# Optimization experiments

Measured on AMD Instinct MI355X. Metric: run time of the kernel, lower is better.

Reference implementation:

```python
import jax, jax.numpy as jnp
import numpy as np

N = 100000
E = 200000
SD = 128   # structural_dim
CD = 768   # chemical_dim


def _linear_params(key, fan_in, fan_out):
    kw, kb = jax.random.split(key)
    bound = 1.0 / np.sqrt(fan_in)
    W = jax.random.uniform(kw, (fan_in, fan_out), jnp.float32, -bound, bound)
    b = jax.random.uniform(kb, (fan_out,), jnp.float32, -bound, bound)
    return W, b


def setup_inputs() -> dict:
    key = jax.random.key(0)
    ks = jax.random.split(key, 12)
    z = jax.random.normal(ks[0], (N, SD), jnp.float32)
    chemistry = jax.random.normal(ks[1], (N, CD), jnp.float32)
    edge = jax.random.randint(ks[2], (E, 2), 0, N, jnp.int64)
    smiles_mask = jax.random.randint(ks[3], (N,), 0, 2, jnp.int32)
    # structural_mlp: SD -> SD//2 -> 1
    sw1, sb1 = _linear_params(ks[4], SD, SD // 2)
    sw2, sb2 = _linear_params(ks[5], SD // 2, 1)
    # chemical_mlp: CD -> CD//4 -> 1
    cw1, cb1 = _linear_params(ks[6], CD, CD // 4)
    cw2, cb2 = _linear_params(ks[7], CD // 4, 1)
    # combined_mlp: SD+CD -> SD -> 1
    mw1, mb1 = _linear_params(ks[8], SD + CD, SD)
    mw2, mb2 = _linear_params(ks[9], SD, 1)
    path_weights = jnp.ones((3,), jnp.float32) / 3.0
    return dict(z=z, chemistry=chemistry, edge=edge, smiles_mask=smiles_mask,
                sw1=sw1, sb1=sb1, sw2=sw2, sb2=sb2,
                cw1=cw1, cb1=cb1, cw2=cw2, cb2=cb2,
                mw1=mw1, mb1=mb1, mw2=mw2, mb2=mb2,
                path_weights=path_weights)


def reference(z, chemistry, edge, smiles_mask,
              sw1, sb1, sw2, sb2,
              cw1, cb1, cw2, cb2,
              mw1, mb1, mw2, mb2,
              path_weights):
    src, dst = edge[:, 0], edge[:, 1]
    # per-edge gathers + elementwise products
    structural_prod = z[src] * z[dst]                    # [E, SD]
    chemical_prod = chemistry[src] * chemistry[dst]      # [E, CD]
    # three small MLPs (dropout is identity in eval mode)
    score_structural = (jax.nn.relu(structural_prod @ sw1 + sb1) @ sw2 + sb2)[:, 0]
    score_chemical = (jax.nn.relu(chemical_prod @ cw1 + cb1) @ cw2 + cb2)[:, 0]
    combined_prod = jnp.concatenate([structural_prod, chemical_prod], axis=-1)  # [E, SD+CD]
    score_combined = (jax.nn.relu(combined_prod @ mw1 + mb1) @ mw2 + mb2)[:, 0]
    # fixed learned path weights (use_gating=False)
    w = jax.nn.softmax(path_weights)
    scores = w[0] * score_structural + w[1] * score_chemical + w[2] * score_combined
    # fall back to structural-only score where chemistry is missing on either end
    mask = smiles_mask.astype(z.dtype)
    both_valid = mask[src] * mask[dst]
    return jnp.where(both_valid > 0.5, scores, score_structural)  # [E]
```

## Files before the change

kernel.cpp:

```cpp
#include <hip/hip_runtime.h>


typedef float  f32x4  __attribute__((ext_vector_type(4)));
typedef __bf16 bf16x8 __attribute__((ext_vector_type(8)));
typedef unsigned short u16x4 __attribute__((ext_vector_type(4)));

static_assert(sizeof(bf16x8) == 16, "bf16x8 must be 16B");
static_assert(sizeof(f32x4) == 16, "f32x4 must be 16B");

#define N_NODES 100000
#define E_EDGES 200000
#define KSTEPS  28
#define NOUT    384
#define PTOT    (KSTEPS * NOUT * 32)

#define WS_WHI   0
#define WS_WLO   688128
#define WS_B1    1376256
#define WS_W2    1377792
#define WS_CONST 1379328

__device__ __forceinline__ unsigned short f2bf(float f) {
  unsigned int x = __float_as_uint(f);
  unsigned int r = (x + 0x7FFFu + ((x >> 16) & 1u)) >> 16;
  return (unsigned short)r;
}
__device__ __forceinline__ float bf2f(unsigned short u) {
  return __uint_as_float(((unsigned int)u) << 16);
}

__global__ __launch_bounds__(256) void prep_kernel(
    const float* __restrict__ sw1, const float* __restrict__ sb1,
    const float* __restrict__ sw2, const float* __restrict__ sb2,
    const float* __restrict__ cw1, const float* __restrict__ cb1,
    const float* __restrict__ cw2, const float* __restrict__ cb2,
    const float* __restrict__ mw1, const float* __restrict__ mb1,
    const float* __restrict__ mw2, const float* __restrict__ mb2,
    const float* __restrict__ pw,  const int* __restrict__ edge_i32,
    unsigned short* __restrict__ whi, unsigned short* __restrict__ wlo,
    float* __restrict__ b1cat, float* __restrict__ w2cat,
    float* __restrict__ consts)
{
  const int idx = blockIdx.x * 256 + threadIdx.x;
  if (idx < PTOT) {
    const int p  = idx / (NOUT * 32);
    const int r  = idx % (NOUT * 32);
    const int n  = r >> 5;
    const int kk = r & 31;
    const int k  = p * 32 + kk;
    float v;
    if (n < 64)       v = (k < 128)  ? sw1[k * 64 + n] : 0.0f;
    else if (n < 256) v = (k >= 128) ? cw1[(size_t)(k - 128) * 192 + (n - 64)] : 0.0f;
    else              v = mw1[(size_t)k * 128 + (n - 256)];
    const unsigned short hi = f2bf(v);
    const unsigned short lo = f2bf(v - bf2f(hi));
    whi[idx] = hi;
    wlo[idx] = lo;
  } else if (idx < PTOT + NOUT) {
    const int j = idx - PTOT;
    float b, w;
    if (j < 64)       { b = sb1[j];       w = sw2[j]; }
    else if (j < 256) { b = cb1[j - 64];  w = cw2[j - 64]; }
    else              { b = mb1[j - 256]; w = mw2[j - 256]; }
    b1cat[j] = b;
    w2cat[j] = w;
  } else if (idx == PTOT + NOUT) {
    const float p0 = pw[0], p1 = pw[1], p2 = pw[2];
    const float mx = fmaxf(p0, fmaxf(p1, p2));
    const float e0 = __expf(p0 - mx), e1 = __expf(p1 - mx), e2 = __expf(p2 - mx);
    const float inv = 1.0f / (e0 + e1 + e2);
    const float w0 = e0 * inv, w1 = e1 * inv, w2v = e2 * inv;
    consts[0] = w0; consts[1] = w1; consts[2] = w2v;
    consts[3] = w0 * sb2[0] + w1 * cb2[0] + w2v * mb2[0];
    consts[4] = sb2[0];
    unsigned o = 0;
    for (int i = 0; i < 64; ++i) o |= (unsigned)edge_i32[2 * i + 1];
    consts[5] = (o == 0u) ? 1.0f : 0.0f;
  }
}

__global__ __launch_bounds__(256, 2) void decoder_main(
    const float* __restrict__ z, const float* __restrict__ chem,
    const int* __restrict__ edge, const int* __restrict__ mask,
    const unsigned short* __restrict__ whi, const unsigned short* __restrict__ wlo,
    const float* __restrict__ b1cat, const float* __restrict__ w2cat,
    const float* __restrict__ consts, float* __restrict__ out)
{
  __shared__ unsigned short Ah[2][64][40];
  __shared__ unsigned short Al[2][64][40];
  __shared__ int   srcL[64];
  __shared__ int   dstL[64];
  __shared__ float validL[64];
  __shared__ float scoreL[64];

  const int tid  = threadIdx.x;
  const int lane = tid & 63;
  const int wv   = tid >> 6;
  const int li   = lane & 15;
  const int q    = lane >> 4;
  const int m0   = blockIdx.x << 6;

  if (tid < 64) {
    scoreL[tid] = 0.0f;
    const int e = m0 + tid;
    int s_, d_;
    if (consts[5] > 0.5f) { s_ = edge[4 * e]; d_ = edge[4 * e + 2]; }
    else                  { s_ = edge[2 * e]; d_ = edge[2 * e + 1]; }
    srcL[tid] = s_;
    dstL[tid] = d_;
    validL[tid] = (mask[s_] != 0 && mask[d_] != 0) ? 1.0f : 0.0f;
  }
  __syncthreads();

  const int mA = tid >> 3;
  const int mB = 32 + mA;
  const int kc = (tid & 7) << 2;
  const float* zsA = z + (size_t)srcL[mA] * 128 + kc;
  const float* zdA = z + (size_t)dstL[mA] * 128 + kc;
  const float* zsB = z + (size_t)srcL[mB] * 128 + kc;
  const float* zdB = z + (size_t)dstL[mB] * 128 + kc;
  const float* csA = chem + (size_t)srcL[mA] * 768 + kc;
  const float* cdA = chem + (size_t)dstL[mA] * 768 + kc;
  const float* csB = chem + (size_t)srcL[mB] * 768 + kc;
  const float* cdB = chem + (size_t)dstL[mB] * 768 + kc;

  auto split_store = [&](int buf, int m, f32x4 p) {
    u16x4 h, l;
#pragma unroll
    for (int j = 0; j < 4; ++j) {
      const unsigned short hj = f2bf(p[j]);
      h[j] = hj;
      l[j] = f2bf(p[j] - bf2f(hj));
    }
    *(u16x4*)&Ah[buf][m][kc] = h;
    *(u16x4*)&Al[buf][m][kc] = l;
  };

  {
    const f32x4 a0 = *(const f32x4*)zsA;
    const f32x4 b0 = *(const f32x4*)zdA;
    const f32x4 a1 = *(const f32x4*)zsB;
    const f32x4 b1 = *(const f32x4*)zdB;
    split_store(0, mA, a0 * b0);
    split_store(0, mB, a1 * b1);
  }
  __syncthreads();

  f32x4 acc[4][6];
#pragma unroll
  for (int mt = 0; mt < 4; ++mt)
#pragma unroll
    for (int i = 0; i < 6; ++i)
      acc[mt][i] = (f32x4){0.f, 0.f, 0.f, 0.f};

  for (int s = 0; s < KSTEPS; ++s) {
    const int buf = s & 1;

    bf16x8 afh[4], afl[4];
#pragma unroll
    for (int mt = 0; mt < 4; ++mt) {
      afh[mt] = *(const bf16x8*)&Ah[buf][mt * 16 + li][q * 8];
      afl[mt] = *(const bf16x8*)&Al[buf][mt * 16 + li][q * 8];
    }

    bf16x8 bfh[6], bfl[6];
    bool act[6];
#pragma unroll
    for (int i = 0; i < 6; ++i) {
      const int ti = wv + 4 * i;
      const int path = (ti < 4) ? 0 : (ti < 16 ? 1 : 2);
      act[i] = (path == 0) ? (s < 4) : (path == 1) ? (s >= 4) : true;
      if (act[i]) {
        const size_t off = (size_t)s * (NOUT * 32) + (size_t)(ti * 16 + li) * 32 + q * 8;
        bfh[i] = *(const bf16x8*)(whi + off);
        bfl[i] = *(const bf16x8*)(wlo + off);
      }
    }

    f32x4 ga, gb, gc, gd;
    if (s + 1 < KSTEPS) {
      const int k0 = (s + 1) * 32;
      if (k0 < 128) {
        ga = *(const f32x4*)(zsA + k0); gb = *(const f32x4*)(zdA + k0);
        gc = *(const f32x4*)(zsB + k0); gd = *(const f32x4*)(zdB + k0);
      } else {
        const int ko = k0 - 128;
        ga = *(const f32x4*)(csA + ko); gb = *(const f32x4*)(cdA + ko);
        gc = *(const f32x4*)(csB + ko); gd = *(const f32x4*)(cdB + ko);
      }
    }

#pragma unroll
    for (int i = 0; i < 6; ++i) {
      if (act[i]) {
#pragma unroll
        for (int mt = 0; mt < 4; ++mt) {
          acc[mt][i] = __builtin_amdgcn_mfma_f32_16x16x32_bf16(afh[mt], bfh[i], acc[mt][i], 0, 0, 0);
          acc[mt][i] = __builtin_amdgcn_mfma_f32_16x16x32_bf16(afh[mt], bfl[i], acc[mt][i], 0, 0, 0);
          acc[mt][i] = __builtin_amdgcn_mfma_f32_16x16x32_bf16(afl[mt], bfh[i], acc[mt][i], 0, 0, 0);
        }
      }
    }

    if (s + 1 < KSTEPS) {
      const int nbuf = buf ^ 1;
      split_store(nbuf, mA, ga * gb);
      split_store(nbuf, mB, gc * gd);
    }
    __syncthreads();
  }

  float part[4][4];
#pragma unroll
  for (int mt = 0; mt < 4; ++mt)
#pragma unroll
    for (int r = 0; r < 4; ++r) part[mt][r] = 0.f;

  const float w0c = consts[0], w1c = consts[1], w2c = consts[2];
#pragma unroll
  for (int i = 0; i < 6; ++i) {
    const int ti = wv + 4 * i;
    const int path = (ti < 4) ? 0 : (ti < 16 ? 1 : 2);
    const int col = ti * 16 + li;
    const float b1 = b1cat[col];
    const float w2 = w2cat[col];
    const float wp  = (path == 0) ? w0c : (path == 1) ? w1c : w2c;
    const float p0f = (path == 0) ? 1.0f : 0.0f;
#pragma unroll
    for (int mt = 0; mt < 4; ++mt) {
#pragma unroll
      for (int r = 0; r < 4; ++r) {
        const float valid = validL[mt * 16 + q * 4 + r];
        const float a = p0f + valid * (wp - p0f);
        float v = acc[mt][i][r] + b1;
        v = fmaxf(v, 0.0f);
        part[mt][r] += a * v * w2;
      }
    }
  }

#pragma unroll
  for (int mt = 0; mt < 4; ++mt) {
#pragma unroll
    for (int r = 0; r < 4; ++r) {
      float v = part[mt][r];
      v += __shfl_xor(v, 1);
      v += __shfl_xor(v, 2);
      v += __shfl_xor(v, 4);
      v += __shfl_xor(v, 8);
      if (li == 0) atomicAdd(&scoreL[mt * 16 + q * 4 + r], v);
    }
  }
  __syncthreads();

  if (tid < 64) {
    const float valid = validL[tid];
    const float cadd = consts[4] + valid * (consts[3] - consts[4]);
    out[m0 + tid] = scoreL[tid] + cadd;
  }
}

extern "C" void kernel_launch(void* const* d_in, const int* in_sizes, int n_in,
                              void* d_out, int out_size, void* d_ws, size_t ws_size,
                              hipStream_t stream)
{
  const float* z    = (const float*)d_in[0];
  const float* chem = (const float*)d_in[1];
  const int*   edge = (const int*)d_in[2];
  const int*   mask = (const int*)d_in[3];
  const float* sw1  = (const float*)d_in[4];
  const float* sb1  = (const float*)d_in[5];
  const float* sw2  = (const float*)d_in[6];
  const float* sb2  = (const float*)d_in[7];
  const float* cw1  = (const float*)d_in[8];
  const float* cb1  = (const float*)d_in[9];
  const float* cw2  = (const float*)d_in[10];
  const float* cb2  = (const float*)d_in[11];
  const float* mw1  = (const float*)d_in[12];
  const float* mb1  = (const float*)d_in[13];
  const float* mw2  = (const float*)d_in[14];
  const float* mb2  = (const float*)d_in[15];
  const float* pw   = (const float*)d_in[16];

  char* ws = (char*)d_ws;
  unsigned short* whi = (unsigned short*)(ws + WS_WHI);
  unsigned short* wlo = (unsigned short*)(ws + WS_WLO);
  float* b1cat  = (float*)(ws + WS_B1);
  float* w2cat  = (float*)(ws + WS_W2);
  float* consts = (float*)(ws + WS_CONST);

  const int prep_tasks  = PTOT + NOUT + 64;
  const int prep_blocks = (prep_tasks + 255) / 256;
  prep_kernel<<<prep_blocks, 256, 0, stream>>>(
      sw1, sb1, sw2, sb2, cw1, cb1, cw2, cb2, mw1, mb1, mw2, mb2, pw, edge,
      whi, wlo, b1cat, w2cat, consts);

  decoder_main<<<E_EDGES / 64, 256, 0, stream>>>(
      z, chem, edge, mask, whi, wlo, b1cat, w2cat, consts, (float*)d_out);
}
```

Measured before the change: 761.5 us.

## Rewrite decoder as single-wave fp16 split-A kernel without LDS staging

```diff
diff --git a/kernel.cpp b/kernel.cpp
--- a/kernel.cpp
+++ b/kernel.cpp
@@ -1,33 +1,19 @@
 #include <hip/hip_runtime.h>
 
 
-typedef float  f32x4  __attribute__((ext_vector_type(4)));
-typedef __bf16 bf16x8 __attribute__((ext_vector_type(8)));
-typedef unsigned short u16x4 __attribute__((ext_vector_type(4)));
-
-static_assert(sizeof(bf16x8) == 16, "bf16x8 must be 16B");
-static_assert(sizeof(f32x4) == 16, "f32x4 must be 16B");
-
-#define N_NODES 100000
+typedef float    f32x4 __attribute__((ext_vector_type(4)));
+typedef _Float16 f16x8 __attribute__((ext_vector_type(8)));
+
 #define E_EDGES 200000
 #define KSTEPS  28
 #define NOUT    384
 #define PTOT    (KSTEPS * NOUT * 32)
-
-#define WS_WHI   0
-#define WS_WLO   688128
-#define WS_B1    1376256
-#define WS_W2    1377792
-#define WS_CONST 1379328
-
-__device__ __forceinline__ unsigned short f2bf(float f) {
-  unsigned int x = __float_as_uint(f);
-  unsigned int r = (x + 0x7FFFu + ((x >> 16) & 1u)) >> 16;
-  return (unsigned short)r;
-}
-__device__ __forceinline__ float bf2f(unsigned short u) {
-  return __uint_as_float(((unsigned int)u) << 16);
-}
+#define PANEL   (NOUT * 32)
+
+#define WS_WH    0
+#define WS_B1    688128
+#define WS_W2    (688128 + 1536)
+#define WS_CONST (688128 + 3072)
 
 __global__ __launch_bounds__(256) void prep_kernel(
     const float* __restrict__ sw1, const float* __restrict__ sb1,
@@ -37,14 +23,14 @@
     const float* __restrict__ mw1, const float* __restrict__ mb1,
     const float* __restrict__ mw2, const float* __restrict__ mb2,
     const float* __restrict__ pw,  const int* __restrict__ edge_i32,
-    unsigned short* __restrict__ whi, unsigned short* __restrict__ wlo,
+    _Float16* __restrict__ wh,
     float* __restrict__ b1cat, float* __restrict__ w2cat,
     float* __restrict__ consts)
 {
   const int idx = blockIdx.x * 256 + threadIdx.x;
   if (idx < PTOT) {
-    const int p  = idx / (NOUT * 32);
-    const int r  = idx % (NOUT * 32);
+    const int p  = idx / PANEL;
+    const int r  = idx % PANEL;
     const int n  = r >> 5;
     const int kk = r & 31;
     const int k  = p * 32 + kk;
@@ -52,10 +38,7 @@
     if (n < 64)       v = (k < 128)  ? sw1[k * 64 + n] : 0.0f;
     else if (n < 256) v = (k >= 128) ? cw1[(size_t)(k - 128) * 192 + (n - 64)] : 0.0f;
     else              v = mw1[(size_t)k * 128 + (n - 256)];
-    const unsigned short hi = f2bf(v);
-    const unsigned short lo = f2bf(v - bf2f(hi));
-    whi[idx] = hi;
-    wlo[idx] = lo;
+    wh[idx] = (_Float16)v;
   } else if (idx < PTOT + NOUT) {
     const int j = idx - PTOT;
     float b, w;
@@ -79,184 +62,213 @@
   }
 }
 
-__global__ __launch_bounds__(256, 2) void decoder_main(
+#define FMA2(ACC, AH, AL, B)                                              \
+  ACC = __builtin_amdgcn_mfma_f32_16x16x32_f16(AH, B, ACC, 0, 0, 0);      \
+  ACC = __builtin_amdgcn_mfma_f32_16x16x32_f16(AL, B, ACC, 0, 0, 0);
+
+__global__ __launch_bounds__(64, 2) void decoder_main(
     const float* __restrict__ z, const float* __restrict__ chem,
     const int* __restrict__ edge, const int* __restrict__ mask,
-    const unsigned short* __restrict__ whi, const unsigned short* __restrict__ wlo,
+    const _Float16* __restrict__ wh,
     const float* __restrict__ b1cat, const float* __restrict__ w2cat,
     const float* __restrict__ consts, float* __restrict__ out)
 {
-  __shared__ unsigned short Ah[2][64][40];
-  __shared__ unsigned short Al[2][64][40];
-  __shared__ int   srcL[64];
-  __shared__ int   dstL[64];
-  __shared__ float validL[64];
-  __shared__ float scoreL[64];
-
-  const int tid  = threadIdx.x;
-  const int lane = tid & 63;
-  const int wv   = tid >> 6;
+  const int lane = threadIdx.x;
   const int li   = lane & 15;
   const int q    = lane >> 4;
-  const int m0   = blockIdx.x << 6;
-
-  if (tid < 64) {
-    scoreL[tid] = 0.0f;
-    const int e = m0 + tid;
-    int s_, d_;
-    if (consts[5] > 0.5f) { s_ = edge[4 * e]; d_ = edge[4 * e + 2]; }
-    else                  { s_ = edge[2 * e]; d_ = edge[2 * e + 1]; }
-    srcL[tid] = s_;
-    dstL[tid] = d_;
-    validL[tid] = (mask[s_] != 0 && mask[d_] != 0) ? 1.0f : 0.0f;
-  }
-  __syncthreads();
-
-  const int mA = tid >> 3;
-  const int mB = 32 + mA;
-  const int kc = (tid & 7) << 2;
-  const float* zsA = z + (size_t)srcL[mA] * 128 + kc;
-  const float* zdA = z + (size_t)dstL[mA] * 128 + kc;
-  const float* zsB = z + (size_t)srcL[mB] * 128 + kc;
-  const float* zdB = z + (size_t)dstL[mB] * 128 + kc;
-  const float* csA = chem + (size_t)srcL[mA] * 768 + kc;
-  const float* cdA = chem + (size_t)dstL[mA] * 768 + kc;
-  const float* csB = chem + (size_t)srcL[mB] * 768 + kc;
-  const float* cdB = chem + (size_t)dstL[mB] * 768 + kc;
-
-  auto split_store = [&](int buf, int m, f32x4 p) {
-    u16x4 h, l;
-#pragma unroll
-    for (int j = 0; j < 4; ++j) {
-      const unsigned short hj = f2bf(p[j]);
-      h[j] = hj;
-      l[j] = f2bf(p[j] - bf2f(hj));
-    }
-    *(u16x4*)&Ah[buf][m][kc] = h;
-    *(u16x4*)&Al[buf][m][kc] = l;
-  };
-
-  {
-    const f32x4 a0 = *(const f32x4*)zsA;
-    const f32x4 b0 = *(const f32x4*)zdA;
-    const f32x4 a1 = *(const f32x4*)zsB;
-    const f32x4 b1 = *(const f32x4*)zdB;
-    split_store(0, mA, a0 * b0);
-    split_store(0, mB, a1 * b1);
-  }
-  __syncthreads();
-
-  f32x4 acc[4][6];
-#pragma unroll
-  for (int mt = 0; mt < 4; ++mt)
-#pragma unroll
-    for (int i = 0; i < 6; ++i)
-      acc[mt][i] = (f32x4){0.f, 0.f, 0.f, 0.f};
-
-  for (int s = 0; s < KSTEPS; ++s) {
-    const int buf = s & 1;
-
-    bf16x8 afh[4], afl[4];
-#pragma unroll
-    for (int mt = 0; mt < 4; ++mt) {
-      afh[mt] = *(const bf16x8*)&Ah[buf][mt * 16 + li][q * 8];
-      afl[mt] = *(const bf16x8*)&Al[buf][mt * 16 + li][q * 8];
-    }
-
-    bf16x8 bfh[6], bfl[6];
-    bool act[6];
-#pragma unroll
-    for (int i = 0; i < 6; ++i) {
-      const int ti = wv + 4 * i;
-      const int path = (ti < 4) ? 0 : (ti < 16 ? 1 : 2);
-      act[i] = (path == 0) ? (s < 4) : (path == 1) ? (s >= 4) : true;
-      if (act[i]) {
-        const size_t off = (size_t)s * (NOUT * 32) + (size_t)(ti * 16 + li) * 32 + q * 8;
-        bfh[i] = *(const bf16x8*)(whi + off);
-        bfl[i] = *(const bf16x8*)(wlo + off);
+  const int kq   = q * 8;
+  const int base = blockIdx.x * 32;
+
+  const int e0 = base + li;
+  const int e1 = base + 16 + li;
+  int s0, d0, s1, d1;
+  if (consts[5] > 0.5f) {
+    s0 = edge[4 * e0]; d0 = edge[4 * e0 + 2];
+    s1 = edge[4 * e1]; d1 = edge[4 * e1 + 2];
+  } else {
+    s0 = edge[2 * e0]; d0 = edge[2 * e0 + 1];
+    s1 = edge[2 * e1]; d1 = edge[2 * e1 + 1];
+  }
+  const float v0 = (mask[s0] != 0 && mask[d0] != 0) ? 1.0f : 0.0f;
+  const float v1 = (mask[s1] != 0 && mask[d1] != 0) ? 1.0f : 0.0f;
+
+  const float* zs0 = z + (size_t)s0 * 128 + kq;
+  const float* zd0 = z + (size_t)d0 * 128 + kq;
+  const float* zs1 = z + (size_t)s1 * 128 + kq;
+  const float* zd1 = z + (size_t)d1 * 128 + kq;
+  const float* cs0 = chem + (size_t)s0 * 768 + kq;
+  const float* cd0 = chem + (size_t)d0 * 768 + kq;
+  const float* cs1 = chem + (size_t)s1 * 768 + kq;
+  const float* cd1 = chem + (size_t)d1 * 768 + kq;
+
+  f32x4 gs0a, gs0b, gd0a, gd0b, gs1a, gs1b, gd1a, gd1b;
+#define LD8(P, OFF, A, B)                        \
+  A = *(const f32x4*)((P) + (OFF));              \
+  B = *(const f32x4*)((P) + (OFF) + 4);
+
+#define MKFRAG(SA, SB, DA, DB, AH, AL)           \
+  {                                              \
+    _Pragma("unroll")                            \
+    for (int j = 0; j < 4; ++j) {                \
+      const float p  = (SA)[j] * (DA)[j];        \
+      const _Float16 h = (_Float16)p;            \
+      (AH)[j] = h;                               \
+      (AL)[j] = (_Float16)(p - (float)h);        \
+      const float p2 = (SB)[j] * (DB)[j];        \
+      const _Float16 h2 = (_Float16)p2;          \
+      (AH)[4 + j] = h2;                          \
+      (AL)[4 + j] = (_Float16)(p2 - (float)h2);  \
+    }                                            \
+  }
+
+#define BFRAG(S, TI) \
+  (*(const f16x8*)(wh + (size_t)(S) * PANEL + ((TI) * 16 + li) * 32 + q * 8))
+
+  const float w0c = consts[0], w1c = consts[1], w2c = consts[2];
+
+  float part[2][4];
+#pragma unroll
+  for (int mt = 0; mt < 2; ++mt)
+#pragma unroll
+    for (int r = 0; r < 4; ++r) part[mt][r] = 0.0f;
+
+#define RETIRE(ACC, TI, MT, WVALID, WINVALID)                              \
+  {                                                                        \
+    const int col = (TI) * 16 + li;                                        \
+    const float b1 = b1cat[col];                                           \
+    const float w2 = w2cat[col];                                           \
+    _Pragma("unroll")                                                      \
+    for (int r = 0; r < 4; ++r) {                                          \
+      const float vld = __shfl((MT) ? v1 : v0, q * 4 + r);                 \
+      const float a = (WINVALID) + vld * ((WVALID) - (WINVALID));          \
+      part[MT][r] += a * fmaxf((ACC)[r] + b1, 0.0f) * w2;                  \
+    }                                                                      \
+  }
+
+  f32x4 accS[4][2], accC[8][2];
+#pragma unroll
+  for (int t = 0; t < 4; ++t) {
+    accS[t][0] = (f32x4){0.f, 0.f, 0.f, 0.f};
+    accS[t][1] = (f32x4){0.f, 0.f, 0.f, 0.f};
+  }
+#pragma unroll
+  for (int t = 0; t < 8; ++t) {
+    accC[t][0] = (f32x4){0.f, 0.f, 0.f, 0.f};
+    accC[t][1] = (f32x4){0.f, 0.f, 0.f, 0.f};
+  }
+
+  LD8(zs0, 0, gs0a, gs0b) LD8(zd0, 0, gd0a, gd0b)
+  LD8(zs1, 0, gs1a, gs1b) LD8(zd1, 0, gd1a, gd1b)
+
+#pragma unroll
+  for (int s = 0; s < 4; ++s) {
+    f16x8 a0h, a0l, a1h, a1l;
+    MKFRAG(gs0a, gs0b, gd0a, gd0b, a0h, a0l)
+    MKFRAG(gs1a, gs1b, gd1a, gd1b, a1h, a1l)
+
+    if (s < 3) {
+      const int off = (s + 1) * 32;
+      LD8(zs0, off, gs0a, gs0b) LD8(zd0, off, gd0a, gd0b)
+      LD8(zs1, off, gs1a, gs1b) LD8(zd1, off, gd1a, gd1b)
+    } else {
+      LD8(cs0, 0, gs0a, gs0b) LD8(cd0, 0, gd0a, gd0b)
+      LD8(cs1, 0, gs1a, gs1b) LD8(cd1, 0, gd1a, gd1b)
+    }
+
+#pragma unroll
+    for (int t = 0; t < 4; ++t) {
+      const f16x8 b = BFRAG(s, t);
+      FMA2(accS[t][0], a0h, a0l, b)
+      FMA2(accS[t][1], a1h, a1l, b)
+    }
+#pragma unroll
+    for (int t = 0; t < 8; ++t) {
+      const f16x8 b = BFRAG(s, 16 + t);
+      FMA2(accC[t][0], a0h, a0l, b)
+      FMA2(accC[t][1], a1h, a1l, b)
+    }
+  }
+
+#pragma unroll
+  for (int t = 0; t < 4; ++t) {
+    RETIRE(accS[t][0], t, 0, w0c, 1.0f)
+    RETIRE(accS[t][1], t, 1, w0c, 1.0f)
+  }
+
+  f32x4 accH[12][2];
+#pragma unroll
+  for (int t = 0; t < 12; ++t) {
+    accH[t][0] = (f32x4){0.f, 0.f, 0.f, 0.f};
+    accH[t][1] = (f32x4){0.f, 0.f, 0.f, 0.f};
+  }
+
+  for (int s = 4; s < KSTEPS; ++s) {
+    f16x8 a0h, a0l, a1h, a1l;
+    MKFRAG(gs0a, gs0b, gd0a, gd0b, a0h, a0l)
+    MKFRAG(gs1a, gs1b, gd1a, gd1b, a1h, a1l)
+
+    if (s + 1 < KSTEPS) {
+      const int off = (s + 1) * 32 - 128;
+      LD8(cs0, off, gs0a, gs0b) LD8(cd0, off, gd0a, gd0b)
+      LD8(cs1, off, gs1a, gs1b) LD8(cd1, off, gd1a, gd1b)
+    }
+
+#pragma unroll
+    for (int t = 0; t < 12; ++t) {
+      const f16x8 b = BFRAG(s, 4 + t);
+      FMA2(accH[t][0], a0h, a0l, b)
+      FMA2(accH[t][1], a1h, a1l, b)
+    }
+#pragma unroll
+    for (int t = 0; t < 8; ++t) {
+      const f16x8 b = BFRAG(s, 16 + t);
+      FMA2(accC[t][0], a0h, a0l, b)
+      FMA2(accC[t][1], a1h, a1l, b)
+    }
+  }
+
+#pragma unroll
+  for (int t = 0; t < 12; ++t) {
+    RETIRE(accH[t][0], 4 + t, 0, w1c, 0.0f)
+    RETIRE(accH[t][1], 4 + t, 1, w1c, 0.0f)
+  }
+#pragma unroll
+  for (int t = 0; t < 8; ++t) {
+    RETIRE(accC[t][0], 16 + t, 0, w2c, 0.0f)
+    RETIRE(accC[t][1], 16 + t, 1, w2c, 0.0f)
+  }
+
+#pragma unroll
+  for (int mt = 0; mt < 2; ++mt) {
+#pragma unroll
+    for (int r = 0; r < 4; ++r) {
+      float vv = part[mt][r];
+      vv += __shfl_xor(vv, 1);
+      vv += __shfl_xor(vv, 2);
+      vv += __shfl_xor(vv, 4);
+      vv += __shfl_xor(vv, 8);
+      part[mt][r] = vv;
+    }
+  }
+
+  const float c3 = consts[3], c4 = consts[4];
+  float outv[2][4];
+#pragma unroll
+  for (int mt = 0; mt < 2; ++mt) {
+#pragma unroll
+    for (int r = 0; r < 4; ++r) {
+      const float vld = __shfl(mt ? v1 : v0, q * 4 + r);
+      outv[mt][r] = part[mt][r] + c4 + vld * (c3 - c4);
+    }
+  }
+  if (li == 0) {
+#pragma unroll
+    for (int mt = 0; mt < 2; ++mt) {
+#pragma unroll
+      for (int r = 0; r < 4; ++r) {
+        out[base + mt * 16 + q * 4 + r] = outv[mt][r];
       }
     }
-
-    f32x4 ga, gb, gc, gd;
-    if (s + 1 < KSTEPS) {
-      const int k0 = (s + 1) * 32;
-      if (k0 < 128) {
-        ga = *(const f32x4*)(zsA + k0); gb = *(const f32x4*)(zdA + k0);
-        gc = *(const f32x4*)(zsB + k0); gd = *(const f32x4*)(zdB + k0);
-      } else {
-        const int ko = k0 - 128;
-        ga = *(const f32x4*)(csA + ko); gb = *(const f32x4*)(cdA + ko);
-        gc = *(const f32x4*)(csB + ko); gd = *(const f32x4*)(cdB + ko);
-      }
-    }
-
-#pragma unroll
-    for (int i = 0; i < 6; ++i) {
-      if (act[i]) {
-#pragma unroll
-        for (int mt = 0; mt < 4; ++mt) {
-          acc[mt][i] = __builtin_amdgcn_mfma_f32_16x16x32_bf16(afh[mt], bfh[i], acc[mt][i], 0, 0, 0);
-          acc[mt][i] = __builtin_amdgcn_mfma_f32_16x16x32_bf16(afh[mt], bfl[i], acc[mt][i], 0, 0, 0);
-          acc[mt][i] = __builtin_amdgcn_mfma_f32_16x16x32_bf16(afl[mt], bfh[i], acc[mt][i], 0, 0, 0);
-        }
-      }
-    }
-
-    if (s + 1 < KSTEPS) {
-      const int nbuf = buf ^ 1;
-      split_store(nbuf, mA, ga * gb);
-      split_store(nbuf, mB, gc * gd);
-    }
-    __syncthreads();
-  }
-
-  float part[4][4];
-#pragma unroll
-  for (int mt = 0; mt < 4; ++mt)
-#pragma unroll
-    for (int r = 0; r < 4; ++r) part[mt][r] = 0.f;
-
-  const float w0c = consts[0], w1c = consts[1], w2c = consts[2];
-#pragma unroll
-  for (int i = 0; i < 6; ++i) {
-    const int ti = wv + 4 * i;
-    const int path = (ti < 4) ? 0 : (ti < 16 ? 1 : 2);
-    const int col = ti * 16 + li;
-    const float b1 = b1cat[col];
-    const float w2 = w2cat[col];
-    const float wp  = (path == 0) ? w0c : (path == 1) ? w1c : w2c;
-    const float p0f = (path == 0) ? 1.0f : 0.0f;
-#pragma unroll
-    for (int mt = 0; mt < 4; ++mt) {
-#pragma unroll
-      for (int r = 0; r < 4; ++r) {
-        const float valid = validL[mt * 16 + q * 4 + r];
-        const float a = p0f + valid * (wp - p0f);
-        float v = acc[mt][i][r] + b1;
-        v = fmaxf(v, 0.0f);
-        part[mt][r] += a * v * w2;
-      }
-    }
-  }
-
-#pragma unroll
-  for (int mt = 0; mt < 4; ++mt) {
-#pragma unroll
-    for (int r = 0; r < 4; ++r) {
-      float v = part[mt][r];
-      v += __shfl_xor(v, 1);
-      v += __shfl_xor(v, 2);
-      v += __shfl_xor(v, 4);
-      v += __shfl_xor(v, 8);
-      if (li == 0) atomicAdd(&scoreL[mt * 16 + q * 4 + r], v);
-    }
-  }
-  __syncthreads();
-
-  if (tid < 64) {
-    const float valid = validL[tid];
-    const float cadd = consts[4] + valid * (consts[3] - consts[4]);
-    out[m0 + tid] = scoreL[tid] + cadd;
   }
 }
 
@@ -283,8 +295,7 @@
   const float* pw   = (const float*)d_in[16];
 
   char* ws = (char*)d_ws;
-  unsigned short* whi = (unsigned short*)(ws + WS_WHI);
-  unsigned short* wlo = (unsigned short*)(ws + WS_WLO);
+  _Float16* wh  = (_Float16*)(ws + WS_WH);
   float* b1cat  = (float*)(ws + WS_B1);
   float* w2cat  = (float*)(ws + WS_W2);
   float* consts = (float*)(ws + WS_CONST);
@@ -293,8 +304,8 @@
   const int prep_blocks = (prep_tasks + 255) / 256;
   prep_kernel<<<prep_blocks, 256, 0, stream>>>(
       sw1, sb1, sw2, sb2, cw1, cb1, cw2, cb2, mw1, mb1, mw2, mb2, pw, edge,
-      whi, wlo, b1cat, w2cat, consts);
-
-  decoder_main<<<E_EDGES / 64, 256, 0, stream>>>(
-      z, chem, edge, mask, whi, wlo, b1cat, w2cat, consts, (float*)d_out);
+      wh, b1cat, w2cat, consts);
+
+  decoder_main<<<E_EDGES / 32, 64, 0, stream>>>(
+      z, chem, edge, mask, wh, b1cat, w2cat, consts, (float*)d_out);
 }
```

After: 1.253 ms. +64.6%, slower.
